# Performance work log

Measured on AMD Instinct MI355X. Metric: run time of the kernel, lower is better.

Reference implementation:

```python
import jax, jax.numpy as jnp
import numpy as np

PROCESS_INIT = 1.0
OBSERVATION_INIT = 1.0


def _build_dynamics_A(K, fut_len):
    # shift-structured single-modal A: state slot i takes value of slot i+1, last step repeats
    sd = 2 * fut_len
    a = np.zeros((sd, sd), dtype=np.float32)
    for i in range(fut_len - 1):
        a[2 * i, 2 * i + 2] = 1.0
        a[2 * i + 1, 2 * i + 3] = 1.0
    a[sd - 2, sd - 2] = 1.0
    a[sd - 1, sd - 1] = 1.0
    # block-diagonal over K modes
    return jnp.asarray(np.kron(np.eye(K, dtype=np.float32), a))


def setup_inputs() -> dict:
    key = jax.random.key(0)
    ks = jax.random.split(key, 6)
    B, A, K, fut_len = 2, 32, 6, 30
    D = K * 2 * fut_len  # 360
    belief_mean = jax.random.normal(ks[0], (B, A, D), dtype=jnp.float32)
    M = jax.random.normal(ks[1], (B, A, D, D), dtype=jnp.float32)
    # symmetric, SPD (eigenvalues ~ 2 +/- 0.2) so linear solves are well-posed
    belief_covariance = 0.003 * (M + jnp.swapaxes(M, -1, -2)) + 2.0 * jnp.eye(D, dtype=jnp.float32)
    observations = jax.random.normal(ks[2], (B, A, D), dtype=jnp.float32)
    rs = jax.random.uniform(ks[3], (B, A), dtype=jnp.float32)
    initialized = jax.random.bernoulli(ks[4], 0.7, (B, A))
    selected = jax.random.bernoulli(ks[5], 0.8, (B, A))
    return {
        "belief_mean": belief_mean,
        "belief_covariance": belief_covariance,
        "observations": observations,
        "rs": rs,
        "initialized": initialized,
        "selected": selected,
        "K": K,
        "fut_len": fut_len,
    }


def reference(belief_mean, belief_covariance, observations, rs, initialized, selected, K, fut_len):
    D = K * 2 * fut_len
    A = _build_dynamics_A(K, fut_len)  # [D, D], static sparse shift structure
    I = jnp.eye(D, dtype=belief_mean.dtype)
    r_obs = (rs + OBSERVATION_INIT)[..., None, None]  # [B, A, 1, 1]

    init_new = selected & (~initialized)  # first observation of agent
    upd = selected & initialized          # predict + Kalman update

    # --- initialization branch ---
    mean_init = observations
    cov_init = belief_covariance + r_obs * I

    # --- predict step: m <- A m ; P <- A P A^T + Q, Q = process_init * I ---
    m_pred = belief_mean @ A.T  # [B, A, D]
    P_pred = jnp.einsum('ij,bnjk,lk->bnil', A, belief_covariance, A) + PROCESS_INIT * I

    # --- update step (H = I): S = P + R ; Kg = P S^{-1} ---
    S = P_pred + r_obs * I
    Kg = P_pred @ jnp.linalg.inv(S)
    m_upd = m_pred + jnp.einsum('bnij,bnj->bni', Kg, observations - m_pred)
    P_upd = (I - Kg) @ P_pred

    # --- scatter the three branches back (masked merge) ---
    mean_out = jnp.where(init_new[..., None], mean_init,
               jnp.where(upd[..., None], m_upd, belief_mean))
    cov_out = jnp.where(init_new[..., None, None], cov_init,
              jnp.where(upd[..., None, None], P_upd, belief_covariance))
    initialized_out = initialized | selected
    return mean_out, cov_out, initialized_out
```

## Files before the change

kernel.cpp:

```cpp
#include <hip/hip_runtime.h>

#define D 360
#define NAG 64
#define NB 60
#define NPAN 6
#define STRD 68
#define COV_OFF (NAG * D)
#define INIT_OFF (COV_OFF + NAG * D * D)
#define RBOFF(par, ag, ct) ((((par) * NAG + (ag)) * 6 + (ct)) * 3600)
#define BVOFF(ag) (2764800 + (ag) * 3600)

__device__ __forceinline__ int gshift(int i) {
    return ((i % 60) < 58) ? (i + 2) : i;
}

__global__ __launch_bounds__(384) void build_kernel(
    const float* __restrict__ P, const float* __restrict__ mean_in,
    const float* __restrict__ obs, const float* __restrict__ rs,
    const int* __restrict__ init_f, const int* __restrict__ sel_f,
    float* __restrict__ out, float* __restrict__ rb)
{
    const int by = blockIdx.x, ag = blockIdx.y, t = threadIdx.x;
    const bool ini = init_f[ag] != 0, sel = sel_f[ag] != 0;
    const float c = rs[ag] + 1.0f;
    if (by == 45) {
        if (t < D) {
            float v = (sel && !ini) ? obs[ag * D + t] : mean_in[ag * D + t];
            out[ag * D + t] = v;
        }
        if (t == 0) out[INIT_OFF + ag] = (ini || sel) ? 1.0f : 0.0f;
        return;
    }
    if (t >= D) return;
    const float* Pa = P + (size_t)ag * D * D;
    float* cov = out + COV_OFF + (size_t)ag * D * D;
    const int j = t;
    if (sel && ini) {
        const int gj = gshift(j);
        #pragma unroll
        for (int s = 0; s < 8; ++s) {
            const int i = by * 8 + s;
            float v = Pa[(size_t)gshift(i) * D + gj];
            if (i == j) v += 1.0f + c;
            cov[(size_t)i * D + j] = v;
            if (i < NB)
                rb[RBOFF(0, ag, j / NB) + i * NB + (j % NB)] = v;
        }
    } else if (sel) {
        #pragma unroll
        for (int s = 0; s < 8; ++s) {
            const int i = by * 8 + s;
            cov[(size_t)i * D + j] = Pa[(size_t)i * D + j] + ((i == j) ? c : 0.0f);
        }
    } else {
        #pragma unroll
        for (int s = 0; s < 8; ++s) {
            const int i = by * 8 + s;
            cov[(size_t)i * D + j] = Pa[(size_t)i * D + j];
        }
    }
}

__device__ __forceinline__ void inv4(float4& m0, float4& m1, float4& m2, float4& m3)
{
    float pv, f;
    pv = 1.0f / m0.x;
    m0.y *= pv; m0.z *= pv; m0.w *= pv; m0.x = pv;
    f = m1.x; m1.y = fmaf(-f, m0.y, m1.y); m1.z = fmaf(-f, m0.z, m1.z); m1.w = fmaf(-f, m0.w, m1.w); m1.x = -f * pv;
    f = m2.x; m2.y = fmaf(-f, m0.y, m2.y); m2.z = fmaf(-f, m0.z, m2.z); m2.w = fmaf(-f, m0.w, m2.w); m2.x = -f * pv;
    f = m3.x; m3.y = fmaf(-f, m0.y, m3.y); m3.z = fmaf(-f, m0.z, m3.z); m3.w = fmaf(-f, m0.w, m3.w); m3.x = -f * pv;
    pv = 1.0f / m1.y;
    m1.x *= pv; m1.z *= pv; m1.w *= pv; m1.y = pv;
    f = m0.y; m0.x = fmaf(-f, m1.x, m0.x); m0.z = fmaf(-f, m1.z, m0.z); m0.w = fmaf(-f, m1.w, m0.w); m0.y = -f * pv;
    f = m2.y; m2.x = fmaf(-f, m1.x, m2.x); m2.z = fmaf(-f, m1.z, m2.z); m2.w = fmaf(-f, m1.w, m2.w); m2.y = -f * pv;
    f = m3.y; m3.x = fmaf(-f, m1.x, m3.x); m3.z = fmaf(-f, m1.z, m3.z); m3.w = fmaf(-f, m1.w, m3.w); m3.y = -f * pv;
    pv = 1.0f / m2.z;
    m2.x *= pv; m2.y *= pv; m2.w *= pv; m2.z = pv;
    f = m0.z; m0.x = fmaf(-f, m2.x, m0.x); m0.y = fmaf(-f, m2.y, m0.y); m0.w = fmaf(-f, m2.w, m0.w); m0.z = -f * pv;
    f = m1.z; m1.x = fmaf(-f, m2.x, m1.x); m1.y = fmaf(-f, m2.y, m1.y); m1.w = fmaf(-f, m2.w, m1.w); m1.z = -f * pv;
    f = m3.z; m3.x = fmaf(-f, m2.x, m3.x); m3.y = fmaf(-f, m2.y, m3.y); m3.w = fmaf(-f, m2.w, m3.w); m3.z = -f * pv;
    pv = 1.0f / m3.w;
    m3.x *= pv; m3.y *= pv; m3.z *= pv; m3.w = pv;
    f = m0.w; m0.x = fmaf(-f, m3.x, m0.x); m0.y = fmaf(-f, m3.y, m0.y); m0.z = fmaf(-f, m3.z, m0.z); m0.w = -f * pv;
    f = m1.w; m1.x = fmaf(-f, m3.x, m1.x); m1.y = fmaf(-f, m3.y, m1.y); m1.z = fmaf(-f, m3.z, m1.z); m1.w = -f * pv;
    f = m2.w; m2.x = fmaf(-f, m3.x, m2.x); m2.y = fmaf(-f, m3.y, m2.y); m2.z = fmaf(-f, m3.z, m2.z); m2.w = -f * pv;
}

__device__ __forceinline__ void lds_gj_inverse(float (&Bsh)[NB][STRD],
                                               float (&praw)[4][STRD], int t)
{
    const int r = t >> 2;
    const int qt = t & 3;
    for (int kb = 0; kb < 15; ++kb) {
        for (int idx = t; idx < 240; idx += 256)
            praw[idx / 60][idx % 60] = Bsh[4 * kb + idx / 60][idx % 60];
        __syncthreads();
        float4 m0 = make_float4(praw[0][4*kb], praw[0][4*kb+1], praw[0][4*kb+2], praw[0][4*kb+3]);
        float4 m1 = make_float4(praw[1][4*kb], praw[1][4*kb+1], praw[1][4*kb+2], praw[1][4*kb+3]);
        float4 m2 = make_float4(praw[2][4*kb], praw[2][4*kb+1], praw[2][4*kb+2], praw[2][4*kb+3]);
        float4 m3 = make_float4(praw[3][4*kb], praw[3][4*kb+1], praw[3][4*kb+2], praw[3][4*kb+3]);
        inv4(m0, m1, m2, m3);
        if (r < NB) {
            const int rel = r - 4 * kb;
            const bool ispiv = (rel >= 0 && rel < 4);
            float4 sc;
            if (ispiv) {
                sc = (rel == 0) ? m0 : (rel == 1) ? m1 : (rel == 2) ? m2 : m3;
            } else {
                const float4 fr = make_float4(Bsh[r][4*kb], Bsh[r][4*kb+1],
                                              Bsh[r][4*kb+2], Bsh[r][4*kb+3]);
                sc.x = -(fr.x * m0.x + fr.y * m1.x + fr.z * m2.x + fr.w * m3.x);
                sc.y = -(fr.x * m0.y + fr.y * m1.y + fr.z * m2.y + fr.w * m3.y);
                sc.z = -(fr.x * m0.z + fr.y * m1.z + fr.z * m2.z + fr.w * m3.z);
                sc.w = -(fr.x * m0.w + fr.y * m1.w + fr.z * m2.w + fr.w * m3.w);
            }
            #pragma unroll
            for (int cc = 0; cc < 15; ++cc) {
                const int col = qt * 15 + cc;
                const int pc = col - 4 * kb;
                if (pc >= 0 && pc < 4) {
                    Bsh[r][col] = (pc == 0) ? sc.x : (pc == 1) ? sc.y : (pc == 2) ? sc.z : sc.w;
                } else {
                    const float base = ispiv ? 0.0f : Bsh[r][col];
                    Bsh[r][col] = fmaf(sc.x, praw[0][col], fmaf(sc.y, praw[1][col],
                                  fmaf(sc.z, praw[2][col], fmaf(sc.w, praw[3][col], base))));
                }
            }
        }
        __syncthreads();
    }
}

__global__ __launch_bounds__(256) void diag0_kernel(
    const int* __restrict__ init_f, const int* __restrict__ sel_f,
    float* __restrict__ rb)
{
    const int ag = blockIdx.x;
    if (!(init_f[ag] && sel_f[ag])) return;
    const int t = threadIdx.x;
    __shared__ float Bsh[NB][STRD];
    __shared__ float praw[4][STRD];
    const float* bsrc = rb + RBOFF(0, ag, 0);
    for (int idx = t; idx < 900; idx += 256) {
        const int r = idx / 15, q = idx % 15;
        *(float4*)&Bsh[r][4 * q] = *(const float4*)(bsrc + r * NB + 4 * q);
    }
    __syncthreads();
    lds_gj_inverse(Bsh, praw, t);
    float* bdst = rb + BVOFF(ag);
    for (int idx = t; idx < 900; idx += 256) {
        const int r = idx / 15, q = idx % 15;
        *(float4*)(bdst + r * NB + 4 * q) = *(const float4*)&Bsh[r][4 * q];
    }
}

__device__ __forceinline__ void mm_row(const float4 a, const float4 b0, const float4 b1,
                                       const float4 b2, const float4 b3, float acc[4]) {
    acc[0] = fmaf(a.x, b0.x, fmaf(a.y, b1.x, fmaf(a.z, b2.x, fmaf(a.w, b3.x, acc[0]))));
    acc[1] = fmaf(a.x, b0.y, fmaf(a.y, b1.y, fmaf(a.z, b2.y, fmaf(a.w, b3.y, acc[1]))));
    acc[2] = fmaf(a.x, b0.z, fmaf(a.y, b1.z, fmaf(a.z, b2.z, fmaf(a.w, b3.z, acc[2]))));
    acc[3] = fmaf(a.x, b0.w, fmaf(a.y, b1.w, fmaf(a.z, b2.w, fmaf(a.w, b3.w, acc[3]))));
}

__global__ __launch_bounds__(256) void pass_kernel(
    float* __restrict__ out, const float* __restrict__ rs,
    const int* __restrict__ init_f, const int* __restrict__ sel_f,
    float* __restrict__ rb, int p)
{
    const int ag = blockIdx.x;
    if (!(init_f[ag] && sel_f[ag])) return;
    const int rt = blockIdx.y;
    const int zc = blockIdx.z;
    float* M = out + COV_OFF + (size_t)ag * D * D;
    const float c = rs[ag] + 1.0f;
    const float c2 = c * c;
    const int t = threadIdx.x;
    const bool special = (p < NPAN - 1) && (rt == p + 1) && (zc == ((p + 1) >> 1));
    __shared__ float Bsh[NB][STRD];
    __shared__ float Fsh[NB][STRD];
    __shared__ float Rsh[NB][STRD];
    __shared__ float praw[4][STRD];

    {
        const float* bsrc = rb + BVOFF(ag);
        for (int idx = t; idx < 900; idx += 256) {
            const int r = idx / 15, q = idx % 15;
            *(float4*)&Bsh[r][4 * q] = *(const float4*)(bsrc + r * NB + 4 * q);
        }
    }
    __syncthreads();

    const int tx = t % 16, ty = t / 16;
    if (rt == p) {
        for (int idx = t; idx < 900; idx += 256) {
            const int r = idx / 15, q = idx % 15;
            *(float4*)&Fsh[r][4 * q] = *(const float4*)&Bsh[r][4 * q];
        }
    } else {
        const float sgn = (rt < p) ? 1.0f : -1.0f;
        const float* rsrc = rb + RBOFF(p & 1, ag, rt);
        for (int idx = t; idx < 900; idx += 256) {
            const int k = idx / 15, q = idx % 15;
            *(float4*)&Rsh[k][4 * q] = *(const float4*)(rsrc + k * NB + 4 * q);
        }
        __syncthreads();
        if (tx < 15 && ty < 15) {
            float acc[4][4];
            #pragma unroll
            for (int i = 0; i < 4; ++i)
                #pragma unroll
                for (int j = 0; j < 4; ++j) acc[i][j] = 0.0f;
            for (int kq = 0; kq < 15; ++kq) {
                #pragma unroll
                for (int m = 0; m < 4; ++m) {
                    const float a0 = Rsh[4*kq+m][4*ty+0];
                    const float a1 = Rsh[4*kq+m][4*ty+1];
                    const float a2 = Rsh[4*kq+m][4*ty+2];
                    const float a3 = Rsh[4*kq+m][4*ty+3];
                    const float4 b = *(const float4*)&Bsh[4*kq+m][4*tx];
                    acc[0][0] = fmaf(a0, b.x, acc[0][0]); acc[0][1] = fmaf(a0, b.y, acc[0][1]);
                    acc[0][2] = fmaf(a0, b.z, acc[0][2]); acc[0][3] = fmaf(a0, b.w, acc[0][3]);
                    acc[1][0] = fmaf(a1, b.x, acc[1][0]); acc[1][1] = fmaf(a1, b.y, acc[1][1]);
                    acc[1][2] = fmaf(a1, b.z, acc[1][2]); acc[1][3] = fmaf(a1, b.w, acc[1][3]);
                    acc[2][0] = fmaf(a2, b.x, acc[2][0]); acc[2][1] = fmaf(a2, b.y, acc[2][1]);
                    acc[2][2] = fmaf(a2, b.z, acc[2][2]); acc[2][3] = fmaf(a2, b.w, acc[2][3]);
                    acc[3][0] = fmaf(a3, b.x, acc[3][0]); acc[3][1] = fmaf(a3, b.y, acc[3][1]);
                    acc[3][2] = fmaf(a3, b.z, acc[3][2]); acc[3][3] = fmaf(a3, b.w, acc[3][3]);
                }
            }
            #pragma unroll
            for (int i = 0; i < 4; ++i) {
                float4 v = make_float4(sgn * acc[i][0], sgn * acc[i][1],
                                       sgn * acc[i][2], sgn * acc[i][3]);
                *(float4*)&Fsh[4 * ty + i][4 * tx] = v;
            }
        }
    }
    __syncthreads();

    for (int jj = 2 * zc; jj < 2 * zc + 2; ++jj) {
        if (jj == 0) {
            for (int idx = t; idx < 900; idx += 256) {
                const int r = idx / 15, q = idx % 15;
                float4 v = *(const float4*)&Fsh[r][4 * q];
                const int rg = rt * NB + r;
                float* dst = M + (size_t)rg * D + p * NB + 4 * q;
                if (p == NPAN - 1) {
                    const int cg = p * NB + 4 * q;
                    float4 o;
                    o.x = ((rg == cg + 0) ? c : 0.f) - c2 * v.x;
                    o.y = ((rg == cg + 1) ? c : 0.f) - c2 * v.y;
                    o.z = ((rg == cg + 2) ? c : 0.f) - c2 * v.z;
                    o.w = ((rg == cg + 3) ? c : 0.f) - c2 * v.w;
                    *(float4*)dst = o;
                } else {
                    *(float4*)dst = v;
                    if (rt == p + 1)
                        *(float4*)(rb + RBOFF((p + 1) & 1, ag, p) + r * NB + 4 * q) = v;
                }
            }
        } else {
            const int ci = jj - 1;
            const int ct = ci + (ci >= p ? 1 : 0);
            __syncthreads();
            const float* rsrc = rb + RBOFF(p & 1, ag, ct);
            for (int idx = t; idx < 900; idx += 256) {
                const int k = idx / 15, q = idx % 15;
                *(float4*)&Rsh[k][4 * q] = *(const float4*)(rsrc + k * NB + 4 * q);
            }
            __syncthreads();
            if (tx < 15 && ty < 15) {
                float acc[4][4];
                #pragma unroll
                for (int i = 0; i < 4; ++i)
                    #pragma unroll
                    for (int j = 0; j < 4; ++j) acc[i][j] = 0.0f;
                for (int kq = 0; kq < 15; ++kq) {
                    float4 a0 = *(const float4*)&Fsh[4 * ty + 0][4 * kq];
                    float4 a1 = *(const float4*)&Fsh[4 * ty + 1][4 * kq];
                    float4 a2 = *(const float4*)&Fsh[4 * ty + 2][4 * kq];
                    float4 a3 = *(const float4*)&Fsh[4 * ty + 3][4 * kq];
                    float4 b0 = *(const float4*)&Rsh[4 * kq + 0][4 * tx];
                    float4 b1 = *(const float4*)&Rsh[4 * kq + 1][4 * tx];
                    float4 b2 = *(const float4*)&Rsh[4 * kq + 2][4 * tx];
                    float4 b3 = *(const float4*)&Rsh[4 * kq + 3][4 * tx];
                    mm_row(a0, b0, b1, b2, b3, acc[0]);
                    mm_row(a1, b0, b1, b2, b3, acc[1]);
                    mm_row(a2, b0, b1, b2, b3, acc[2]);
                    mm_row(a3, b0, b1, b2, b3, acc[3]);
                }
                #pragma unroll
                for (int i = 0; i < 4; ++i) {
                    const int rg = rt * NB + 4 * ty + i;
                    float* dst = M + (size_t)rg * D + ct * NB + 4 * tx;
                    float4 base;
                    if (rt == p) { base = make_float4(0.f, 0.f, 0.f, 0.f); }
                    else         { base = *(const float4*)dst; }
                    float4 v;
                    v.x = base.x + acc[i][0];
                    v.y = base.y + acc[i][1];
                    v.z = base.z + acc[i][2];
                    v.w = base.w + acc[i][3];
                    if (p < NPAN - 1) {
                        if (rt == p + 1) {
                            float* rdst = rb + RBOFF((p + 1) & 1, ag, ct)
                                        + (4 * ty + i) * NB + 4 * tx;
                            *(float4*)rdst = v;
                        }
                        *(float4*)dst = v;
                        if (special && ct == p + 1)
                            *(float4*)&Bsh[4 * ty + i][4 * tx] = v;
                    } else {
                        const int cg = ct * NB + 4 * tx;
                        float4 o;
                        o.x = ((rg == cg + 0) ? c : 0.f) - c2 * v.x;
                        o.y = ((rg == cg + 1) ? c : 0.f) - c2 * v.y;
                        o.z = ((rg == cg + 2) ? c : 0.f) - c2 * v.z;
                        o.w = ((rg == cg + 3) ? c : 0.f) - c2 * v.w;
                        *(float4*)dst = o;
                    }
                }
            }
        }
    }

    if (special) {
        __syncthreads();
        lds_gj_inverse(Bsh, praw, t);
        float* bdst = rb + BVOFF(ag);
        for (int idx = t; idx < 900; idx += 256) {
            const int r = idx / 15, q = idx % 15;
            *(float4*)(bdst + r * NB + 4 * q) = *(const float4*)&Bsh[r][4 * q];
        }
    }
}

__global__ __launch_bounds__(384) void solve_mean_kernel(
    float* __restrict__ out, const float* __restrict__ mean_in,
    const float* __restrict__ obs, const float* __restrict__ rs,
    const int* __restrict__ init_f, const int* __restrict__ sel_f)
{
    const int ag = blockIdx.x;
    if (!(init_f[ag] && sel_f[ag])) return;
    const float* C = out + COV_OFF + (size_t)ag * D * D;
    __shared__ float dsh[D];
    const int t = threadIdx.x;
    if (t < D) dsh[t] = obs[ag * D + t] - mean_in[ag * D + gshift(t)];
    __syncthreads();
    if (t < D) {
        float dot = 0.0f;
        #pragma unroll 8
        for (int j = 0; j < D; ++j)
            dot = fmaf(C[(size_t)j * D + t], dsh[j], dot);
        const float c = rs[ag] + 1.0f;
        out[ag * D + t] = obs[ag * D + t] - dsh[t] + dot / c;
    }
}

extern "C" void kernel_launch(void* const* d_in, const int* in_sizes, int n_in,
                              void* d_out, int out_size, void* d_ws, size_t ws_size,
                              hipStream_t stream) {
    const float* mean_in     = (const float*)d_in[0];
    const float* P           = (const float*)d_in[1];
    const float* obs         = (const float*)d_in[2];
    const float* rs          = (const float*)d_in[3];
    const int*   initialized = (const int*)d_in[4];
    const int*   selected    = (const int*)d_in[5];
    float* out = (float*)d_out;
    float* rb  = (float*)d_ws;

    build_kernel<<<dim3(46, NAG), 384, 0, stream>>>(P, mean_in, obs, rs,
                                                    initialized, selected, out, rb);
    diag0_kernel<<<NAG, 256, 0, stream>>>(initialized, selected, rb);
    for (int p = 0; p < NPAN; ++p)
        pass_kernel<<<dim3(NAG, NPAN, 3), 256, 0, stream>>>(out, rs, initialized,
                                                            selected, rb, p);
    solve_mean_kernel<<<NAG, 384, 0, stream>>>(out, mean_in, obs, rs, initialized, selected);
}
```

Measured before the change: 336.8 us.

## Fuse all stages into one persistent kernel with per-agent spin barriers

Replaces the build, diag0, six pass launches and the mean solve with one kernel. Each agent is handled by 12 workgroups that synchronize through atomic counter/generation barriers in workspace memory, which removes the launch overhead and inter-kernel gaps. Each workgroup now handles three column tiles per pass instead of two, and the build phase uses float4 copies for the non-updated agents. The spin barriers depend on all 768 workgroups being resident at once, which the launch bound of 3 blocks per CU is meant to ensure. The final mean solve runs on a single workgroup per agent with 256 threads.

```diff
diff --git a/kernel.cpp b/kernel.cpp
--- a/kernel.cpp
+++ b/kernel.cpp
@@ -5,60 +5,33 @@
 #define NB 60
 #define NPAN 6
 #define STRD 68
+#define WPA 12
 #define COV_OFF (NAG * D)
 #define INIT_OFF (COV_OFF + NAG * D * D)
 #define RBOFF(par, ag, ct) ((((par) * NAG + (ag)) * 6 + (ct)) * 3600)
 #define BVOFF(ag) (2764800 + (ag) * 3600)
+#define SYNC_OFF 3000000
 
 __device__ __forceinline__ int gshift(int i) {
     return ((i % 60) < 58) ? (i + 2) : i;
 }
 
-__global__ __launch_bounds__(384) void build_kernel(
-    const float* __restrict__ P, const float* __restrict__ mean_in,
-    const float* __restrict__ obs, const float* __restrict__ rs,
-    const int* __restrict__ init_f, const int* __restrict__ sel_f,
-    float* __restrict__ out, float* __restrict__ rb)
-{
-    const int by = blockIdx.x, ag = blockIdx.y, t = threadIdx.x;
-    const bool ini = init_f[ag] != 0, sel = sel_f[ag] != 0;
-    const float c = rs[ag] + 1.0f;
-    if (by == 45) {
-        if (t < D) {
-            float v = (sel && !ini) ? obs[ag * D + t] : mean_in[ag * D + t];
-            out[ag * D + t] = v;
-        }
-        if (t == 0) out[INIT_OFF + ag] = (ini || sel) ? 1.0f : 0.0f;
-        return;
-    }
-    if (t >= D) return;
-    const float* Pa = P + (size_t)ag * D * D;
-    float* cov = out + COV_OFF + (size_t)ag * D * D;
-    const int j = t;
-    if (sel && ini) {
-        const int gj = gshift(j);
-        #pragma unroll
-        for (int s = 0; s < 8; ++s) {
-            const int i = by * 8 + s;
-            float v = Pa[(size_t)gshift(i) * D + gj];
-            if (i == j) v += 1.0f + c;
-            cov[(size_t)i * D + j] = v;
-            if (i < NB)
-                rb[RBOFF(0, ag, j / NB) + i * NB + (j % NB)] = v;
-        }
-    } else if (sel) {
-        #pragma unroll
-        for (int s = 0; s < 8; ++s) {
-            const int i = by * 8 + s;
-            cov[(size_t)i * D + j] = Pa[(size_t)i * D + j] + ((i == j) ? c : 0.0f);
-        }
-    } else {
-        #pragma unroll
-        for (int s = 0; s < 8; ++s) {
-            const int i = by * 8 + s;
-            cov[(size_t)i * D + j] = Pa[(size_t)i * D + j];
-        }
-    }
+__device__ __forceinline__ void agsync(unsigned* cnt, unsigned* gen) {
+    __syncthreads();
+    if (threadIdx.x == 0) {
+        __threadfence();
+        unsigned g = __hip_atomic_load(gen, __ATOMIC_RELAXED, __HIP_MEMORY_SCOPE_AGENT);
+        unsigned a = __hip_atomic_fetch_add(cnt, 1u, __ATOMIC_ACQ_REL, __HIP_MEMORY_SCOPE_AGENT);
+        if (a == WPA - 1) {
+            __hip_atomic_store(cnt, 0u, __ATOMIC_RELAXED, __HIP_MEMORY_SCOPE_AGENT);
+            __hip_atomic_fetch_add(gen, 1u, __ATOMIC_RELEASE, __HIP_MEMORY_SCOPE_AGENT);
+        } else {
+            while (__hip_atomic_load(gen, __ATOMIC_ACQUIRE, __HIP_MEMORY_SCOPE_AGENT) == g)
+                __builtin_amdgcn_s_sleep(2);
+        }
+        __threadfence();
+    }
+    __syncthreads();
 }
 
 __device__ __forceinline__ void inv4(float4& m0, float4& m1, float4& m2, float4& m3)
@@ -131,29 +104,6 @@
     }
 }
 
-__global__ __launch_bounds__(256) void diag0_kernel(
-    const int* __restrict__ init_f, const int* __restrict__ sel_f,
-    float* __restrict__ rb)
-{
-    const int ag = blockIdx.x;
-    if (!(init_f[ag] && sel_f[ag])) return;
-    const int t = threadIdx.x;
-    __shared__ float Bsh[NB][STRD];
-    __shared__ float praw[4][STRD];
-    const float* bsrc = rb + RBOFF(0, ag, 0);
-    for (int idx = t; idx < 900; idx += 256) {
-        const int r = idx / 15, q = idx % 15;
-        *(float4*)&Bsh[r][4 * q] = *(const float4*)(bsrc + r * NB + 4 * q);
-    }
-    __syncthreads();
-    lds_gj_inverse(Bsh, praw, t);
-    float* bdst = rb + BVOFF(ag);
-    for (int idx = t; idx < 900; idx += 256) {
-        const int r = idx / 15, q = idx % 15;
-        *(float4*)(bdst + r * NB + 4 * q) = *(const float4*)&Bsh[r][4 * q];
-    }
-}
-
 __device__ __forceinline__ void mm_row(const float4 a, const float4 b0, const float4 b1,
                                        const float4 b2, const float4 b3, float acc[4]) {
     acc[0] = fmaf(a.x, b0.x, fmaf(a.y, b1.x, fmaf(a.z, b2.x, fmaf(a.w, b3.x, acc[0]))));
@@ -162,108 +112,99 @@
     acc[3] = fmaf(a.x, b0.w, fmaf(a.y, b1.w, fmaf(a.z, b2.w, fmaf(a.w, b3.w, acc[3]))));
 }
 
-__global__ __launch_bounds__(256) void pass_kernel(
-    float* __restrict__ out, const float* __restrict__ rs,
+__global__ __launch_bounds__(256, 3) void fused_kernel(
+    const float* __restrict__ P, const float* __restrict__ mean_in,
+    const float* __restrict__ obs, const float* __restrict__ rs,
     const int* __restrict__ init_f, const int* __restrict__ sel_f,
-    float* __restrict__ rb, int p)
+    float* __restrict__ out, float* __restrict__ rb, unsigned* __restrict__ sync)
 {
-    const int ag = blockIdx.x;
-    if (!(init_f[ag] && sel_f[ag])) return;
-    const int rt = blockIdx.y;
-    const int zc = blockIdx.z;
-    float* M = out + COV_OFF + (size_t)ag * D * D;
+    const int wid = blockIdx.x;
+    const int ag = wid / WPA;
+    const int s  = wid % WPA;
+    const int rt = s >> 1;
+    const int h  = s & 1;
+    const int t  = threadIdx.x;
+    const bool ini = init_f[ag] != 0, sel = sel_f[ag] != 0;
+    const bool act = ini && sel;
     const float c = rs[ag] + 1.0f;
     const float c2 = c * c;
-    const int t = threadIdx.x;
-    const bool special = (p < NPAN - 1) && (rt == p + 1) && (zc == ((p + 1) >> 1));
+    const float* Pa = P + (size_t)ag * D * D;
+    float* cov = out + COV_OFF + (size_t)ag * D * D;
+    unsigned* cnt = sync + 16 * ag;
+    unsigned* gen = sync + 16 * ag + 1;
+
     __shared__ float Bsh[NB][STRD];
     __shared__ float Fsh[NB][STRD];
     __shared__ float Rsh[NB][STRD];
     __shared__ float praw[4][STRD];
 
-    {
-        const float* bsrc = rb + BVOFF(ag);
+    if (act) {
+        for (int idx = t; idx < 30 * 360; idx += 256) {
+            const int i = s * 30 + idx / 360, j = idx % 360;
+            float v = Pa[(size_t)gshift(i) * D + gshift(j)];
+            if (i == j) v += 1.0f + c;
+            cov[(size_t)i * D + j] = v;
+            if (i < NB) rb[RBOFF(0, ag, j / 60) + i * 60 + (j % 60)] = v;
+        }
+    } else if (sel) {
+        for (int idx = t; idx < 30 * 90; idx += 256) {
+            const int i = s * 30 + idx / 90, q = idx % 90;
+            float4 v = *(const float4*)(Pa + (size_t)i * D + 4 * q);
+            const int dq = i - 4 * q;
+            if (dq == 0) v.x += c; else if (dq == 1) v.y += c;
+            else if (dq == 2) v.z += c; else if (dq == 3) v.w += c;
+            *(float4*)(cov + (size_t)i * D + 4 * q) = v;
+        }
+    } else {
+        for (int idx = t; idx < 30 * 90; idx += 256) {
+            const int i = s * 30 + idx / 90, q = idx % 90;
+            *(float4*)(cov + (size_t)i * D + 4 * q) =
+                *(const float4*)(Pa + (size_t)i * D + 4 * q);
+        }
+    }
+    if (s == 0) {
+        for (int tt = t; tt < D; tt += 256)
+            out[ag * D + tt] = (sel && !ini) ? obs[ag * D + tt] : mean_in[ag * D + tt];
+        if (t == 0) out[INIT_OFF + ag] = (ini || sel) ? 1.0f : 0.0f;
+    }
+    if (!act) return;
+    agsync(cnt, gen);
+
+    if (s == 0) {
+        const float* bsrc = rb + RBOFF(0, ag, 0);
         for (int idx = t; idx < 900; idx += 256) {
             const int r = idx / 15, q = idx % 15;
             *(float4*)&Bsh[r][4 * q] = *(const float4*)(bsrc + r * NB + 4 * q);
         }
-    }
-    __syncthreads();
-
-    const int tx = t % 16, ty = t / 16;
-    if (rt == p) {
+        __syncthreads();
+        lds_gj_inverse(Bsh, praw, t);
+        float* bdst = rb + BVOFF(ag);
         for (int idx = t; idx < 900; idx += 256) {
             const int r = idx / 15, q = idx % 15;
-            *(float4*)&Fsh[r][4 * q] = *(const float4*)&Bsh[r][4 * q];
-        }
-    } else {
-        const float sgn = (rt < p) ? 1.0f : -1.0f;
-        const float* rsrc = rb + RBOFF(p & 1, ag, rt);
-        for (int idx = t; idx < 900; idx += 256) {
-            const int k = idx / 15, q = idx % 15;
-            *(float4*)&Rsh[k][4 * q] = *(const float4*)(rsrc + k * NB + 4 * q);
-        }
-        __syncthreads();
-        if (tx < 15 && ty < 15) {
-            float acc[4][4];
-            #pragma unroll
-            for (int i = 0; i < 4; ++i)
-                #pragma unroll
-                for (int j = 0; j < 4; ++j) acc[i][j] = 0.0f;
-            for (int kq = 0; kq < 15; ++kq) {
-                #pragma unroll
-                for (int m = 0; m < 4; ++m) {
-                    const float a0 = Rsh[4*kq+m][4*ty+0];
-                    const float a1 = Rsh[4*kq+m][4*ty+1];
-                    const float a2 = Rsh[4*kq+m][4*ty+2];
-                    const float a3 = Rsh[4*kq+m][4*ty+3];
-                    const float4 b = *(const float4*)&Bsh[4*kq+m][4*tx];
-                    acc[0][0] = fmaf(a0, b.x, acc[0][0]); acc[0][1] = fmaf(a0, b.y, acc[0][1]);
-                    acc[0][2] = fmaf(a0, b.z, acc[0][2]); acc[0][3] = fmaf(a0, b.w, acc[0][3]);
-                    acc[1][0] = fmaf(a1, b.x, acc[1][0]); acc[1][1] = fmaf(a1, b.y, acc[1][1]);
-                    acc[1][2] = fmaf(a1, b.z, acc[1][2]); acc[1][3] = fmaf(a1, b.w, acc[1][3]);
-                    acc[2][0] = fmaf(a2, b.x, acc[2][0]); acc[2][1] = fmaf(a2, b.y, acc[2][1]);
-                    acc[2][2] = fmaf(a2, b.z, acc[2][2]); acc[2][3] = fmaf(a2, b.w, acc[2][3]);
-                    acc[3][0] = fmaf(a3, b.x, acc[3][0]); acc[3][1] = fmaf(a3, b.y, acc[3][1]);
-                    acc[3][2] = fmaf(a3, b.z, acc[3][2]); acc[3][3] = fmaf(a3, b.w, acc[3][3]);
-                }
-            }
-            #pragma unroll
-            for (int i = 0; i < 4; ++i) {
-                float4 v = make_float4(sgn * acc[i][0], sgn * acc[i][1],
-                                       sgn * acc[i][2], sgn * acc[i][3]);
-                *(float4*)&Fsh[4 * ty + i][4 * tx] = v;
-            }
-        }
-    }
-    __syncthreads();
-
-    for (int jj = 2 * zc; jj < 2 * zc + 2; ++jj) {
-        if (jj == 0) {
+            *(float4*)(bdst + r * NB + 4 * q) = *(const float4*)&Bsh[r][4 * q];
+        }
+    }
+    agsync(cnt, gen);
+
+    const int tx = t % 16, ty = t / 16;
+    for (int p = 0; p < NPAN; ++p) {
+        const bool special = (p < NPAN - 1) && (rt == p + 1) && (h == ((p + 1) >= 3 ? 1 : 0));
+        {
+            const float* bsrc = rb + BVOFF(ag);
             for (int idx = t; idx < 900; idx += 256) {
                 const int r = idx / 15, q = idx % 15;
-                float4 v = *(const float4*)&Fsh[r][4 * q];
-                const int rg = rt * NB + r;
-                float* dst = M + (size_t)rg * D + p * NB + 4 * q;
-                if (p == NPAN - 1) {
-                    const int cg = p * NB + 4 * q;
-                    float4 o;
-                    o.x = ((rg == cg + 0) ? c : 0.f) - c2 * v.x;
-                    o.y = ((rg == cg + 1) ? c : 0.f) - c2 * v.y;
-                    o.z = ((rg == cg + 2) ? c : 0.f) - c2 * v.z;
-                    o.w = ((rg == cg + 3) ? c : 0.f) - c2 * v.w;
-                    *(float4*)dst = o;
-                } else {
-                    *(float4*)dst = v;
-                    if (rt == p + 1)
-                        *(float4*)(rb + RBOFF((p + 1) & 1, ag, p) + r * NB + 4 * q) = v;
-                }
+                *(float4*)&Bsh[r][4 * q] = *(const float4*)(bsrc + r * NB + 4 * q);
+            }
+        }
+        __syncthreads();
+        if (rt == p) {
+            for (int idx = t; idx < 900; idx += 256) {
+                const int r = idx / 15, q = idx % 15;
+                *(float4*)&Fsh[r][4 * q] = *(const float4*)&Bsh[r][4 * q];
             }
         } else {
-            const int ci = jj - 1;
-            const int ct = ci + (ci >= p ? 1 : 0);
-            __syncthreads();
-            const float* rsrc = rb + RBOFF(p & 1, ag, ct);
+            const float sgn = (rt < p) ? 1.0f : -1.0f;
+            const float* rsrc = rb + RBOFF(p & 1, ag, rt);
             for (int idx = t; idx < 900; idx += 256) {
                 const int k = idx / 15, q = idx % 15;
                 *(float4*)&Rsh[k][4 * q] = *(const float4*)(rsrc + k * NB + 4 * q);
@@ -276,84 +217,140 @@
                     #pragma unroll
                     for (int j = 0; j < 4; ++j) acc[i][j] = 0.0f;
                 for (int kq = 0; kq < 15; ++kq) {
-                    float4 a0 = *(const float4*)&Fsh[4 * ty + 0][4 * kq];
-                    float4 a1 = *(const float4*)&Fsh[4 * ty + 1][4 * kq];
-                    float4 a2 = *(const float4*)&Fsh[4 * ty + 2][4 * kq];
-                    float4 a3 = *(const float4*)&Fsh[4 * ty + 3][4 * kq];
-                    float4 b0 = *(const float4*)&Rsh[4 * kq + 0][4 * tx];
-                    float4 b1 = *(const float4*)&Rsh[4 * kq + 1][4 * tx];
-                    float4 b2 = *(const float4*)&Rsh[4 * kq + 2][4 * tx];
-                    float4 b3 = *(const float4*)&Rsh[4 * kq + 3][4 * tx];
-                    mm_row(a0, b0, b1, b2, b3, acc[0]);
-                    mm_row(a1, b0, b1, b2, b3, acc[1]);
-                    mm_row(a2, b0, b1, b2, b3, acc[2]);
-                    mm_row(a3, b0, b1, b2, b3, acc[3]);
+                    #pragma unroll
+                    for (int m = 0; m < 4; ++m) {
+                        const float a0 = Rsh[4*kq+m][4*ty+0];
+                        const float a1 = Rsh[4*kq+m][4*ty+1];
+                        const float a2 = Rsh[4*kq+m][4*ty+2];
+                        const float a3 = Rsh[4*kq+m][4*ty+3];
+                        const float4 b = *(const float4*)&Bsh[4*kq+m][4*tx];
+                        acc[0][0] = fmaf(a0, b.x, acc[0][0]); acc[0][1] = fmaf(a0, b.y, acc[0][1]);
+                        acc[0][2] = fmaf(a0, b.z, acc[0][2]); acc[0][3] = fmaf(a0, b.w, acc[0][3]);
+                        acc[1][0] = fmaf(a1, b.x, acc[1][0]); acc[1][1] = fmaf(a1, b.y, acc[1][1]);
+                        acc[1][2] = fmaf(a1, b.z, acc[1][2]); acc[1][3] = fmaf(a1, b.w, acc[1][3]);
+                        acc[2][0] = fmaf(a2, b.x, acc[2][0]); acc[2][1] = fmaf(a2, b.y, acc[2][1]);
+                        acc[2][2] = fmaf(a2, b.z, acc[2][2]); acc[2][3] = fmaf(a2, b.w, acc[2][3]);
+                        acc[3][0] = fmaf(a3, b.x, acc[3][0]); acc[3][1] = fmaf(a3, b.y, acc[3][1]);
+                        acc[3][2] = fmaf(a3, b.z, acc[3][2]); acc[3][3] = fmaf(a3, b.w, acc[3][3]);
+                    }
                 }
                 #pragma unroll
-                for (int i = 0; i < 4; ++i) {
-                    const int rg = rt * NB + 4 * ty + i;
-                    float* dst = M + (size_t)rg * D + ct * NB + 4 * tx;
-                    float4 base;
-                    if (rt == p) { base = make_float4(0.f, 0.f, 0.f, 0.f); }
-                    else         { base = *(const float4*)dst; }
-                    float4 v;
-                    v.x = base.x + acc[i][0];
-                    v.y = base.y + acc[i][1];
-                    v.z = base.z + acc[i][2];
-                    v.w = base.w + acc[i][3];
-                    if (p < NPAN - 1) {
-                        if (rt == p + 1) {
-                            float* rdst = rb + RBOFF((p + 1) & 1, ag, ct)
-                                        + (4 * ty + i) * NB + 4 * tx;
-                            *(float4*)rdst = v;
-                        }
-                        *(float4*)dst = v;
-                        if (special && ct == p + 1)
-                            *(float4*)&Bsh[4 * ty + i][4 * tx] = v;
-                    } else {
-                        const int cg = ct * NB + 4 * tx;
+                for (int i = 0; i < 4; ++i)
+                    *(float4*)&Fsh[4 * ty + i][4 * tx] =
+                        make_float4(sgn * acc[i][0], sgn * acc[i][1],
+                                    sgn * acc[i][2], sgn * acc[i][3]);
+            }
+        }
+        __syncthreads();
+
+        for (int jj = 3 * h; jj < 3 * h + 3; ++jj) {
+            if (jj == 0) {
+                for (int idx = t; idx < 900; idx += 256) {
+                    const int r = idx / 15, q = idx % 15;
+                    float4 v = *(const float4*)&Fsh[r][4 * q];
+                    const int rg = rt * NB + r;
+                    float* dst = cov + (size_t)rg * D + p * NB + 4 * q;
+                    if (p == NPAN - 1) {
+                        const int cg = p * NB + 4 * q;
                         float4 o;
                         o.x = ((rg == cg + 0) ? c : 0.f) - c2 * v.x;
                         o.y = ((rg == cg + 1) ? c : 0.f) - c2 * v.y;
                         o.z = ((rg == cg + 2) ? c : 0.f) - c2 * v.z;
                         o.w = ((rg == cg + 3) ? c : 0.f) - c2 * v.w;
                         *(float4*)dst = o;
+                    } else {
+                        *(float4*)dst = v;
+                        if (rt == p + 1)
+                            *(float4*)(rb + RBOFF((p + 1) & 1, ag, p) + r * NB + 4 * q) = v;
                     }
                 }
-            }
-        }
-    }
-
-    if (special) {
-        __syncthreads();
-        lds_gj_inverse(Bsh, praw, t);
-        float* bdst = rb + BVOFF(ag);
-        for (int idx = t; idx < 900; idx += 256) {
-            const int r = idx / 15, q = idx % 15;
-            *(float4*)(bdst + r * NB + 4 * q) = *(const float4*)&Bsh[r][4 * q];
-        }
-    }
-}
-
-__global__ __launch_bounds__(384) void solve_mean_kernel(
-    float* __restrict__ out, const float* __restrict__ mean_in,
-    const float* __restrict__ obs, const float* __restrict__ rs,
-    const int* __restrict__ init_f, const int* __restrict__ sel_f)
-{
-    const int ag = blockIdx.x;
-    if (!(init_f[ag] && sel_f[ag])) return;
-    const float* C = out + COV_OFF + (size_t)ag * D * D;
-    __shared__ float dsh[D];
-    const int t = threadIdx.x;
-    if (t < D) dsh[t] = obs[ag * D + t] - mean_in[ag * D + gshift(t)];
-    __syncthreads();
-    if (t < D) {
-        float dot = 0.0f;
-        #pragma unroll 8
-        for (int j = 0; j < D; ++j)
-            dot = fmaf(C[(size_t)j * D + t], dsh[j], dot);
-        const float c = rs[ag] + 1.0f;
-        out[ag * D + t] = obs[ag * D + t] - dsh[t] + dot / c;
+            } else {
+                const int ci = jj - 1;
+                const int ct = ci + (ci >= p ? 1 : 0);
+                __syncthreads();
+                const float* rsrc = rb + RBOFF(p & 1, ag, ct);
+                for (int idx = t; idx < 900; idx += 256) {
+                    const int k = idx / 15, q = idx % 15;
+                    *(float4*)&Rsh[k][4 * q] = *(const float4*)(rsrc + k * NB + 4 * q);
+                }
+                __syncthreads();
+                if (tx < 15 && ty < 15) {
+                    float acc[4][4];
+                    #pragma unroll
+                    for (int i = 0; i < 4; ++i)
+                        #pragma unroll
+                        for (int j = 0; j < 4; ++j) acc[i][j] = 0.0f;
+                    for (int kq = 0; kq < 15; ++kq) {
+                        float4 a0 = *(const float4*)&Fsh[4 * ty + 0][4 * kq];
+                        float4 a1 = *(const float4*)&Fsh[4 * ty + 1][4 * kq];
+                        float4 a2 = *(const float4*)&Fsh[4 * ty + 2][4 * kq];
+                        float4 a3 = *(const float4*)&Fsh[4 * ty + 3][4 * kq];
+                        float4 b0 = *(const float4*)&Rsh[4 * kq + 0][4 * tx];
+                        float4 b1 = *(const float4*)&Rsh[4 * kq + 1][4 * tx];
+                        float4 b2 = *(const float4*)&Rsh[4 * kq + 2][4 * tx];
+                        float4 b3 = *(const float4*)&Rsh[4 * kq + 3][4 * tx];
+                        mm_row(a0, b0, b1, b2, b3, acc[0]);
+                        mm_row(a1, b0, b1, b2, b3, acc[1]);
+                        mm_row(a2, b0, b1, b2, b3, acc[2]);
+                        mm_row(a3, b0, b1, b2, b3, acc[3]);
+                    }
+                    #pragma unroll
+                    for (int i = 0; i < 4; ++i) {
+                        const int rg = rt * NB + 4 * ty + i;
+                        float* dst = cov + (size_t)rg * D + ct * NB + 4 * tx;
+                        float4 base;
+                        if (rt == p) { base = make_float4(0.f, 0.f, 0.f, 0.f); }
+                        else         { base = *(const float4*)dst; }
+                        float4 v;
+                        v.x = base.x + acc[i][0];
+                        v.y = base.y + acc[i][1];
+                        v.z = base.z + acc[i][2];
+                        v.w = base.w + acc[i][3];
+                        if (p < NPAN - 1) {
+                            if (rt == p + 1) {
+                                *(float4*)(rb + RBOFF((p + 1) & 1, ag, ct)
+                                           + (4 * ty + i) * NB + 4 * tx) = v;
+                            }
+                            *(float4*)dst = v;
+                            if (special && ct == p + 1)
+                                *(float4*)&Bsh[4 * ty + i][4 * tx] = v;
+                        } else {
+                            const int cg = ct * NB + 4 * tx;
+                            float4 o;
+                            o.x = ((rg == cg + 0) ? c : 0.f) - c2 * v.x;
+                            o.y = ((rg == cg + 1) ? c : 0.f) - c2 * v.y;
+                            o.z = ((rg == cg + 2) ? c : 0.f) - c2 * v.z;
+                            o.w = ((rg == cg + 3) ? c : 0.f) - c2 * v.w;
+                            *(float4*)dst = o;
+                        }
+                    }
+                }
+            }
+        }
+        if (special) {
+            __syncthreads();
+            lds_gj_inverse(Bsh, praw, t);
+            float* bdst = rb + BVOFF(ag);
+            for (int idx = t; idx < 900; idx += 256) {
+                const int r = idx / 15, q = idx % 15;
+                *(float4*)(bdst + r * NB + 4 * q) = *(const float4*)&Bsh[r][4 * q];
+            }
+        }
+        agsync(cnt, gen);
+    }
+
+    if (s == 0) {
+        float* dsh = &Fsh[0][0];
+        for (int tt = t; tt < D; tt += 256)
+            dsh[tt] = obs[ag * D + tt] - mean_in[ag * D + gshift(tt)];
+        __syncthreads();
+        for (int tt = t; tt < D; tt += 256) {
+            float dot = 0.0f;
+            #pragma unroll 8
+            for (int j = 0; j < D; ++j)
+                dot = fmaf(cov[(size_t)j * D + tt], dsh[j], dot);
+            out[ag * D + tt] = obs[ag * D + tt] - dsh[tt] + dot / c;
+        }
     }
 }
 
@@ -368,12 +365,9 @@
     const int*   selected    = (const int*)d_in[5];
     float* out = (float*)d_out;
     float* rb  = (float*)d_ws;
-
-    build_kernel<<<dim3(46, NAG), 384, 0, stream>>>(P, mean_in, obs, rs,
-                                                    initialized, selected, out, rb);
-    diag0_kernel<<<NAG, 256, 0, stream>>>(initialized, selected, rb);
-    for (int p = 0; p < NPAN; ++p)
-        pass_kernel<<<dim3(NAG, NPAN, 3), 256, 0, stream>>>(out, rs, initialized,
-                                                            selected, rb, p);
-    solve_mean_kernel<<<NAG, 384, 0, stream>>>(out, mean_in, obs, rs, initialized, selected);
-}
+    unsigned* syncp = (unsigned*)((float*)d_ws + SYNC_OFF);
+
+    hipMemsetAsync(syncp, 0, NAG * 16 * sizeof(unsigned), stream);
+    fused_kernel<<<NAG * WPA, 256, 0, stream>>>(P, mean_in, obs, rs, initialized,
+                                                selected, out, rb, syncp);
+}
```

New measurement: 804.1 us. +138.8%, slower.
